# Performance work log

Measured on AMD Instinct MI355X. Metric: run time of the kernel, lower is better.

The kernel has to match this reference:

```python
import jax, jax.numpy as jnp
import numpy as np

B, D, K = 16384, 256, 1024

def setup_inputs() -> dict:
    key = jax.random.key(0)
    k1, k2 = jax.random.split(key)
    x = jax.random.normal(k1, (B, D), dtype=jnp.float32)
    centers = jax.random.uniform(k2, (K, D), dtype=jnp.float32)  # RandomUniform(0,1)
    betas = jnp.ones((K,), dtype=jnp.float32)
    return {"x": x, "centers": centers, "betas": betas}

def reference(x, centers, betas):
    x_sq = jnp.sum(x * x, axis=-1, keepdims=True)          # [B,1]
    c_sq = jnp.sum(centers * centers, axis=-1)             # [K]
    cross = jnp.einsum('bd,kd->bk', x, centers)            # [B,K]
    diffnorm = x_sq + c_sq[None, :] - 2.0 * cross          # [B,K]
    return jnp.exp(-betas[None, :] * diffnorm)             # [B,K]
```

## Files before the change

kernel.cpp:

```cpp
#include <hip/hip_runtime.h>
#include <stdint.h>

#define D_DIM 256
#define K_CTR 1024
#define B_ROWS 16384
#define BM 32
#define NSTRIP (B_ROWS / BM)

typedef float f32x4 __attribute__((ext_vector_type(4)));
typedef float f32x2 __attribute__((ext_vector_type(2)));
typedef long long i64x2 __attribute__((ext_vector_type(2)));
typedef unsigned int u32x4 __attribute__((ext_vector_type(4)));

static __device__ __forceinline__ unsigned cvt4_fp8(const float4 v) {
    int r = __builtin_amdgcn_cvt_pk_fp8_f32(v.x, v.y, 0, false);
    r = __builtin_amdgcn_cvt_pk_fp8_f32(v.z, v.w, r, true);
    return (unsigned)r;
}

static __device__ __forceinline__ void barrier_lgkm() {
    asm volatile("s_waitcnt lgkmcnt(0)" ::: "memory");
    __builtin_amdgcn_s_barrier();
}

static __device__ __forceinline__ unsigned lane_pos(int l) {
    return (unsigned)((l >> 4) * 64 + ((l >> 1) & 3) * 16 + ((l >> 3) & 1) * 8 + (l & 1) * 4);
}

__global__ __launch_bounds__(256) void rbf_prep(const float* __restrict__ x,
                                                const float* __restrict__ centers,
                                                unsigned char* __restrict__ cbf,
                                                float* __restrict__ csq,
                                                unsigned char* __restrict__ xb,
                                                float* __restrict__ xsq) {
    const int w = threadIdx.x >> 6;
    const int l = threadIdx.x & 63;
    if (blockIdx.x < 2048) {
        #pragma unroll
        for (int i = 0; i < 2; ++i) {
            const int row = blockIdx.x * 8 + i * 4 + w;
            const float4 v = *reinterpret_cast<const float4*>(x + (size_t)row * D_DIM + l * 4);
            float s = v.x * v.x + v.y * v.y + v.z * v.z + v.w * v.w;
            const unsigned u = cvt4_fp8(v);
            const int strip = row >> 5, rloc = row & 31;
            *reinterpret_cast<unsigned*>(xb + (size_t)strip * 8192 + rloc * 256
                + (lane_pos(l) ^ ((unsigned)(rloc & 7) << 4))) = u;
            #pragma unroll
            for (int off = 1; off < 64; off <<= 1) s += __shfl_xor(s, off);
            if (l == 0) xsq[row] = s;
        }
    } else {
        const int c0 = (blockIdx.x - 2048) * 4 + w;
        const float4 v = *reinterpret_cast<const float4*>(centers + c0 * D_DIM + l * 4);
        float s = v.x * v.x + v.y * v.y + v.z * v.z + v.w * v.w;
        const unsigned u = cvt4_fp8(v);
        const unsigned off = (unsigned)((c0 >> 4) * 4096 + (l >> 4) * 1024
                           + (((l >> 1) & 3) * 16 + (c0 & 15)) * 16
                           + ((l >> 3) & 1) * 8 + (l & 1) * 4);
        *reinterpret_cast<unsigned*>(cbf + off) = u;
        #pragma unroll
        for (int off2 = 1; off2 < 64; off2 <<= 1) s += __shfl_xor(s, off2);
        if (l == 0) csq[c0] = s;
    }
}

__global__ __launch_bounds__(512, 4) void rbf_main(const unsigned char* __restrict__ xb,
                                                   const float* __restrict__ xsq,
                                                   const unsigned char* __restrict__ cbf,
                                                   const float* __restrict__ csq,
                                                   const float* __restrict__ betas,
                                                   float* __restrict__ out) {
    __shared__ __align__(16) unsigned char As[BM * D_DIM];
    __shared__ __align__(16) float obuf[2][BM * 128];

    const int tid = threadIdx.x;
    const int w = tid >> 6;
    const int l = tid & 63;
    const int strip = (blockIdx.x & 7) * 64 + (blockIdx.x >> 3);
    const int row0 = strip * BM;

    {
        const u32x4 v = *reinterpret_cast<const u32x4*>(xb + (size_t)strip * 8192 + tid * 16);
        *reinterpret_cast<u32x4*>(As + tid * 16) = v;
    }

    const int hk = l >> 4;
    const int lr = l & 15;
    const unsigned char* bwave = cbf + l * 16;

    i64x2 b0[4], b1[4];
    {
        const unsigned char* bbase = bwave + w * 4096;
        #pragma unroll
        for (int p = 0; p < 4; ++p)
            b0[p] = *reinterpret_cast<const i64x2*>(bbase + p * 1024);
    }
    barrier_lgkm();

    i64x2 a[2][4];
    #pragma unroll
    for (int m = 0; m < 2; ++m) {
        const int r = m * 16 + lr;
        #pragma unroll
        for (int p = 0; p < 4; ++p)
            a[m][p] = *reinterpret_cast<const i64x2*>(
                As + r * 256 + ((unsigned)(p * 64 + hk * 16) ^ ((unsigned)(lr & 7) << 4)));
    }
    const float xs0 = xsq[row0 + lr];
    const float xs1 = xsq[row0 + 16 + lr];
    const float LOG2E = 1.4426950408889634f;

    f32x2 svA[4] = {}, svB[4] = {};

    #pragma unroll
    for (int ph = 0; ph < 8; ++ph) {
        const int colp = ph * 128;
        const i64x2 (&bc)[4] = (ph & 1) ? b1 : b0;
        i64x2 (&bn)[4] = (ph & 1) ? b0 : b1;

        if (ph < 7) {
            const unsigned char* bbase = bwave + ((ph + 1) * 8 + w) * 4096;
            #pragma unroll
            for (int p = 0; p < 4; ++p)
                bn[p] = *reinterpret_cast<const i64x2*>(bbase + p * 1024);
        }

        f32x4 acc[2] = {};
        #pragma unroll
        for (int p = 0; p < 4; ++p)
            #pragma unroll
            for (int m = 0; m < 2; ++m) {
                acc[m] = __builtin_amdgcn_mfma_f32_16x16x32_fp8_fp8(bc[p][0], a[m][p][0], acc[m], 0, 0, 0);
                acc[m] = __builtin_amdgcn_mfma_f32_16x16x32_fp8_fp8(bc[p][1], a[m][p][1], acc[m], 0, 0, 0);
            }

        float* ob = obuf[ph & 1];
        {
            const int cl = w * 16 + hk * 4;
            const f32x4 cs = *reinterpret_cast<const f32x4*>(csq + colp + cl);
            const f32x4 bt = *reinterpret_cast<const f32x4*>(betas + colp + cl);
            #pragma unroll
            for (int m = 0; m < 2; ++m) {
                const int r = m * 16 + lr;
                const float xsv = m ? xs1 : xs0;
                f32x4 rv;
                #pragma unroll
                for (int j = 0; j < 4; ++j) {
                    const float btl2 = bt[j] * LOG2E;
                    const float cc = -btl2 * (xsv + cs[j]);
                    rv[j] = __builtin_exp2f(__builtin_fmaf(btl2 + btl2, acc[m][j], cc));
                }
                *reinterpret_cast<f32x4*>(reinterpret_cast<char*>(ob)
                    + r * 512 + ((unsigned)(cl * 4) ^ ((unsigned)(r & 7) << 4))) = rv;
            }
        }
        barrier_lgkm();

        f32x2 (&sv)[4]  = (ph & 1) ? svB : svA;
        f32x2 (&svo)[4] = (ph & 1) ? svA : svB;
        asm volatile("" :: "v"(svo[0]), "v"(svo[1]), "v"(svo[2]), "v"(svo[3]));
        #pragma unroll
        for (int i = 0; i < 4; ++i) {
            const int r = w * 4 + i;
            sv[i] = *reinterpret_cast<const f32x2*>(reinterpret_cast<const char*>(obuf[ph & 1])
                    + r * 512 + ((unsigned)(l * 8) ^ ((unsigned)(r & 7) << 4)));
        }
        #pragma unroll
        for (int i = 0; i < 4; ++i) {
            const int r = w * 4 + i;
            *reinterpret_cast<f32x2*>(out + (size_t)(row0 + r) * K_CTR + colp + l * 2) = sv[i];
        }
    }
}

extern "C" void kernel_launch(void* const* d_in, const int* in_sizes, int n_in,
                              void* d_out, int out_size, void* d_ws, size_t ws_size,
                              hipStream_t stream) {
    const float* x       = (const float*)d_in[0];
    const float* centers = (const float*)d_in[1];
    const float* betas   = (const float*)d_in[2];
    float* out = (float*)d_out;

    unsigned char* cbf = (unsigned char*)d_ws;
    float* csq = (float*)((char*)d_ws + 262144);
    unsigned char* xb  = (unsigned char*)d_ws + 262144 + 4096;
    float* xsq = (float*)((char*)d_ws + 262144 + 4096 + (size_t)NSTRIP * 8192);

    rbf_prep<<<2048 + K_CTR / 4, 256, 0, stream>>>(x, centers, cbf, csq, xb, xsq);
    rbf_main<<<NSTRIP, 512, 0, stream>>>(xb, xsq, cbf, csq, betas, out);
}
```

Before: 26.55 us.

## Specialize waves into MFMA producers and global-store consumers with double-buffered LDS

Splits the 8 waves of each block into 4 compute waves, each handling two 16-column center tiles per phase, and 4 store waves that drain the previous phase's LDS output buffer to global memory. Output stores are meant to overlap with the next phase's MFMA and exp work, and s_setprio raises the priority of the MFMA sections. In exchange, compute is concentrated on half the waves, which doubles per-wave MFMA work and register pressure. It also adds a trailing store phase after the loop.

```diff
diff --git a/kernel.cpp b/kernel.cpp
--- a/kernel.cpp
+++ b/kernel.cpp
@@ -76,6 +76,7 @@
     const int tid = threadIdx.x;
     const int w = tid >> 6;
     const int l = tid & 63;
+    const bool is_store = (w >= 4);
     const int strip = (blockIdx.x & 7) * 64 + (blockIdx.x >> 3);
     const int row0 = strip * BM;
 
@@ -88,87 +89,111 @@
     const int lr = l & 15;
     const unsigned char* bwave = cbf + l * 16;
 
-    i64x2 b0[4], b1[4];
-    {
-        const unsigned char* bbase = bwave + w * 4096;
+    i64x2 bA[4], bB[4];
+    if (!is_store) {
+        const unsigned char* bbase = bwave + (w * 2) * 4096;
         #pragma unroll
         for (int p = 0; p < 4; ++p)
-            b0[p] = *reinterpret_cast<const i64x2*>(bbase + p * 1024);
+            bA[p] = *reinterpret_cast<const i64x2*>(bbase + p * 1024);
     }
     barrier_lgkm();
 
     i64x2 a[2][4];
-    #pragma unroll
-    for (int m = 0; m < 2; ++m) {
-        const int r = m * 16 + lr;
-        #pragma unroll
-        for (int p = 0; p < 4; ++p)
-            a[m][p] = *reinterpret_cast<const i64x2*>(
-                As + r * 256 + ((unsigned)(p * 64 + hk * 16) ^ ((unsigned)(lr & 7) << 4)));
-    }
-    const float xs0 = xsq[row0 + lr];
-    const float xs1 = xsq[row0 + 16 + lr];
+    float xs0 = 0.f, xs1 = 0.f;
+    if (!is_store) {
+        #pragma unroll
+        for (int m = 0; m < 2; ++m) {
+            const int r = m * 16 + lr;
+            #pragma unroll
+            for (int p = 0; p < 4; ++p)
+                a[m][p] = *reinterpret_cast<const i64x2*>(
+                    As + r * 256 + ((unsigned)(p * 64 + hk * 16) ^ ((unsigned)(lr & 7) << 4)));
+        }
+        xs0 = xsq[row0 + lr];
+        xs1 = xsq[row0 + 16 + lr];
+    }
     const float LOG2E = 1.4426950408889634f;
 
-    f32x2 svA[4] = {}, svB[4] = {};
+    f32x2 svA[8] = {}, svB[8] = {};
+    const int srow = (w - 4) * 8;
 
     #pragma unroll
     for (int ph = 0; ph < 8; ++ph) {
-        const int colp = ph * 128;
-        const i64x2 (&bc)[4] = (ph & 1) ? b1 : b0;
-        i64x2 (&bn)[4] = (ph & 1) ? b0 : b1;
-
-        if (ph < 7) {
-            const unsigned char* bbase = bwave + ((ph + 1) * 8 + w) * 4096;
-            #pragma unroll
-            for (int p = 0; p < 4; ++p)
-                bn[p] = *reinterpret_cast<const i64x2*>(bbase + p * 1024);
-        }
-
-        f32x4 acc[2] = {};
-        #pragma unroll
-        for (int p = 0; p < 4; ++p)
-            #pragma unroll
-            for (int m = 0; m < 2; ++m) {
-                acc[m] = __builtin_amdgcn_mfma_f32_16x16x32_fp8_fp8(bc[p][0], a[m][p][0], acc[m], 0, 0, 0);
-                acc[m] = __builtin_amdgcn_mfma_f32_16x16x32_fp8_fp8(bc[p][1], a[m][p][1], acc[m], 0, 0, 0);
+        if (!is_store) {
+            float* ob = obuf[ph & 1];
+            #pragma unroll
+            for (int e = 0; e < 2; ++e) {
+                if (e == 0) {
+                    const unsigned char* bbase = bwave + (ph * 8 + w * 2 + 1) * 4096;
+                    #pragma unroll
+                    for (int p = 0; p < 4; ++p)
+                        bB[p] = *reinterpret_cast<const i64x2*>(bbase + p * 1024);
+                } else if (ph < 7) {
+                    const unsigned char* bbase = bwave + ((ph + 1) * 8 + w * 2) * 4096;
+                    #pragma unroll
+                    for (int p = 0; p < 4; ++p)
+                        bA[p] = *reinterpret_cast<const i64x2*>(bbase + p * 1024);
+                }
+                const i64x2 (&bc)[4] = e ? bB : bA;
+
+                f32x4 acc[2] = {};
+                __builtin_amdgcn_s_setprio(1);
+                #pragma unroll
+                for (int p = 0; p < 4; ++p)
+                    #pragma unroll
+                    for (int m = 0; m < 2; ++m) {
+                        acc[m] = __builtin_amdgcn_mfma_f32_16x16x32_fp8_fp8(bc[p][0], a[m][p][0], acc[m], 0, 0, 0);
+                        acc[m] = __builtin_amdgcn_mfma_f32_16x16x32_fp8_fp8(bc[p][1], a[m][p][1], acc[m], 0, 0, 0);
+                    }
+                __builtin_amdgcn_s_setprio(0);
+
+                const int cl = (w * 2 + e) * 16 + hk * 4;
+                const f32x4 cs = *reinterpret_cast<const f32x4*>(csq + ph * 128 + cl);
+                const f32x4 bt = *reinterpret_cast<const f32x4*>(betas + ph * 128 + cl);
+                #pragma unroll
+                for (int m = 0; m < 2; ++m) {
+                    const int r = m * 16 + lr;
+                    const float xsv = m ? xs1 : xs0;
+                    f32x4 rv;
+                    #pragma unroll
+                    for (int j = 0; j < 4; ++j) {
+                        const float btl2 = bt[j] * LOG2E;
+                        const float cc = -btl2 * (xsv + cs[j]);
+                        rv[j] = __builtin_exp2f(__builtin_fmaf(btl2 + btl2, acc[m][j], cc));
+                    }
+                    *reinterpret_cast<f32x4*>(reinterpret_cast<char*>(ob)
+                        + r * 512 + ((unsigned)(cl * 4) ^ ((unsigned)(r & 7) << 4))) = rv;
+                }
             }
-
-        float* ob = obuf[ph & 1];
-        {
-            const int cl = w * 16 + hk * 4;
-            const f32x4 cs = *reinterpret_cast<const f32x4*>(csq + colp + cl);
-            const f32x4 bt = *reinterpret_cast<const f32x4*>(betas + colp + cl);
-            #pragma unroll
-            for (int m = 0; m < 2; ++m) {
-                const int r = m * 16 + lr;
-                const float xsv = m ? xs1 : xs0;
-                f32x4 rv;
-                #pragma unroll
-                for (int j = 0; j < 4; ++j) {
-                    const float btl2 = bt[j] * LOG2E;
-                    const float cc = -btl2 * (xsv + cs[j]);
-                    rv[j] = __builtin_exp2f(__builtin_fmaf(btl2 + btl2, acc[m][j], cc));
-                }
-                *reinterpret_cast<f32x4*>(reinterpret_cast<char*>(ob)
-                    + r * 512 + ((unsigned)(cl * 4) ^ ((unsigned)(r & 7) << 4))) = rv;
+        } else if (ph >= 1) {
+            const char* ob = reinterpret_cast<const char*>(obuf[(ph - 1) & 1]);
+            f32x2 (&sv)[8]  = (ph & 1) ? svA : svB;
+            f32x2 (&svo)[8] = (ph & 1) ? svB : svA;
+            asm volatile("" :: "v"(svo[0]), "v"(svo[3]), "v"(svo[5]), "v"(svo[7]));
+            #pragma unroll
+            for (int i = 0; i < 8; ++i) {
+                const int r = srow + i;
+                sv[i] = *reinterpret_cast<const f32x2*>(ob
+                        + r * 512 + ((unsigned)(l * 8) ^ ((unsigned)(r & 7) << 4)));
             }
+            #pragma unroll
+            for (int i = 0; i < 8; ++i) {
+                const int r = srow + i;
+                *reinterpret_cast<f32x2*>(out + (size_t)(row0 + r) * K_CTR
+                        + (ph - 1) * 128 + l * 2) = sv[i];
+            }
         }
         barrier_lgkm();
-
-        f32x2 (&sv)[4]  = (ph & 1) ? svB : svA;
-        f32x2 (&svo)[4] = (ph & 1) ? svA : svB;
-        asm volatile("" :: "v"(svo[0]), "v"(svo[1]), "v"(svo[2]), "v"(svo[3]));
-        #pragma unroll
-        for (int i = 0; i < 4; ++i) {
-            const int r = w * 4 + i;
-            sv[i] = *reinterpret_cast<const f32x2*>(reinterpret_cast<const char*>(obuf[ph & 1])
+    }
+
+    if (is_store) {
+        const char* ob = reinterpret_cast<const char*>(obuf[1]);
+        #pragma unroll
+        for (int i = 0; i < 8; ++i) {
+            const int r = srow + i;
+            const f32x2 v = *reinterpret_cast<const f32x2*>(ob
                     + r * 512 + ((unsigned)(l * 8) ^ ((unsigned)(r & 7) << 4)));
-        }
-        #pragma unroll
-        for (int i = 0; i < 4; ++i) {
-            const int r = w * 4 + i;
-            *reinterpret_cast<f32x2*>(out + (size_t)(row0 + r) * K_CTR + colp + l * 2) = sv[i];
+            *reinterpret_cast<f32x2*>(out + (size_t)(row0 + r) * K_CTR + 7 * 128 + l * 2) = v;
         }
     }
 }
```

Result: slower. 28.71 us (+8.1%).
